# Kernel optimization log

Hardware: AMD Instinct MI355X
Metric: run time of the kernel (lower is better)

Reference implementation:

```python
import jax, jax.numpy as jnp
import numpy as np

N_NODES = 50000
N_EDGES = 1_600_000
IN_C, HID_C, OUT_C = 512, 256, 50
ALPHA = 0.1
NUM_LAYERS = 10


def setup_inputs() -> dict:
    key = jax.random.key(0)
    ks = jax.random.split(key, 8)
    x = jax.random.normal(ks[0], (N_NODES, IN_C), dtype=jnp.float32)
    edge_row = jax.random.randint(ks[1], (N_EDGES,), 0, N_NODES, dtype=jnp.int32)
    edge_col = jax.random.randint(ks[2], (N_EDGES,), 0, N_NODES, dtype=jnp.int32)
    edge_weight = jax.random.uniform(ks[3], (N_EDGES,), dtype=jnp.float32)
    s1 = 1.0 / np.sqrt(IN_C)
    s2 = 1.0 / np.sqrt(HID_C)
    W1 = jax.random.uniform(ks[4], (IN_C, HID_C), minval=-s1, maxval=s1, dtype=jnp.float32)
    b1 = jax.random.uniform(ks[5], (HID_C,), minval=-s1, maxval=s1, dtype=jnp.float32)
    W2 = jax.random.uniform(ks[6], (HID_C, OUT_C), minval=-s2, maxval=s2, dtype=jnp.float32)
    b2 = jax.random.uniform(ks[7], (OUT_C,), minval=-s2, maxval=s2, dtype=jnp.float32)
    return {"x": x, "edge_row": edge_row, "edge_col": edge_col,
            "edge_weight": edge_weight, "W1": W1, "b1": b1, "W2": W2, "b2": b2}


def reference(x, edge_row, edge_col, edge_weight, W1, b1, W2, b2):
    # MLP: Linear -> ReLU -> Linear (dropout inactive in eval, no batch norm)
    h = jax.nn.relu(x @ W1 + b1)          # [N, HID_C]
    h = h @ W2 + b2                        # [N, OUT_C]
    x0 = h

    def spmm(v):
        # out[i] = sum_{e: row[e]==i} w[e] * v[col[e]]
        msgs = v[edge_col] * edge_weight[:, None]   # [E, OUT_C]
        return jax.ops.segment_sum(msgs, edge_row, num_segments=N_NODES)

    def step(h, _):
        h = spmm(h) * (1.0 - ALPHA) + ALPHA * x0
        return h, None

    h, _ = jax.lax.scan(step, h, None, length=NUM_LAYERS)
    return jax.nn.log_softmax(h, axis=1)
```

## Files before the change

### kernel.cpp

```cpp
#include <hip/hip_runtime.h>
#include <cstddef>
#include <cstdint>
#include <math.h>

#define N_NODES 50000
#define N_EDGES 1600000
#define IN_C 512
#define HID_C 256
#define OUT_C 50
#define PAD_C 64
#define NUM_LAYERS 10
#define NBUCK 98
#define BSHIFT 9
#define BCAP 20480
#define PHB_CHUNK 8192
#define PHB_BLOCKS 196
#define AP 40

typedef __attribute__((ext_vector_type(8))) short short8;
typedef __attribute__((ext_vector_type(4))) float floatx4;

__device__ inline unsigned short f2bf(float f) {
    unsigned int u = __float_as_uint(f);
    u += 0x7fffu + ((u >> 16) & 1u);
    return (unsigned short)(u >> 16);
}

__global__ __launch_bounds__(256) void transpose_w1(const float* __restrict__ W1,
                                                    unsigned short* __restrict__ Wt) {
    __shared__ float tile[32][33];
    int bx = blockIdx.x;
    int by = blockIdx.y;
    int tx = threadIdx.x & 31, ty = threadIdx.x >> 5;
#pragma unroll
    for (int i = 0; i < 32; i += 8)
        tile[ty + i][tx] = W1[(bx * 32 + ty + i) * HID_C + by * 32 + tx];
    __syncthreads();
#pragma unroll
    for (int i = 0; i < 32; i += 8)
        Wt[(size_t)(by * 32 + ty + i) * IN_C + bx * 32 + tx] = f2bf(tile[tx][ty + i]);
}

__global__ __launch_bounds__(256) void gemm1_mfma(const float* __restrict__ A,
                                                  const unsigned short* __restrict__ Wt,
                                                  const float* __restrict__ bias,
                                                  float* __restrict__ C) {
    __shared__ unsigned short As[64 * AP];
    __shared__ unsigned short Bs[128 * AP];
    const int tid = threadIdx.x;
    const int wave = tid >> 6, lane = tid & 63;
    const int quad = lane >> 4, l16 = lane & 15;
    const int m0 = blockIdx.x * 64, n0 = blockIdx.y * 128;
    const int wm = (wave >> 1) * 32, wn = (wave & 1) * 64;

    floatx4 acc[2][4];
#pragma unroll
    for (int i = 0; i < 2; ++i)
#pragma unroll
        for (int j = 0; j < 4; ++j) acc[i][j] = (floatx4){0.f, 0.f, 0.f, 0.f};

    const int arow   = tid >> 2;
    const int achunk = (tid & 3) * 8;
    const int brow   = tid >> 1;
    const int bchunk = (tid & 1) * 16;

    float4 pa0[2], pa1[2];
    uint4  pb0[2], pb1[2];

    auto fetch = [&](int k0, float4* pa, uint4* pb) {
        int gr = m0 + arow;
        pa[0] = make_float4(0.f, 0.f, 0.f, 0.f);
        pa[1] = pa[0];
        if (gr < N_NODES) {
            const float* base = A + (size_t)gr * IN_C + k0 + achunk;
            pa[0] = *(const float4*)base;
            pa[1] = *(const float4*)(base + 4);
        }
        const unsigned short* wb = Wt + (size_t)(n0 + brow) * IN_C + k0 + bchunk;
        pb[0] = *(const uint4*)wb;
        pb[1] = *(const uint4*)(wb + 8);
    };
    auto stage = [&](const float4* pa, const uint4* pb) {
        ushort4 u1, u2;
        u1.x = f2bf(pa[0].x); u1.y = f2bf(pa[0].y); u1.z = f2bf(pa[0].z); u1.w = f2bf(pa[0].w);
        u2.x = f2bf(pa[1].x); u2.y = f2bf(pa[1].y); u2.z = f2bf(pa[1].z); u2.w = f2bf(pa[1].w);
        *(ushort4*)&As[arow * AP + achunk]     = u1;
        *(ushort4*)&As[arow * AP + achunk + 4] = u2;
        *(uint4*)&Bs[brow * AP + bchunk]     = pb[0];
        *(uint4*)&Bs[brow * AP + bchunk + 8] = pb[1];
    };
    auto mfma_phase = [&]() {
        short8 af[2], bf[4];
#pragma unroll
        for (int nt = 0; nt < 4; ++nt)
            bf[nt] = *(const short8*)&Bs[(wn + nt * 16 + l16) * AP + quad * 8];
#pragma unroll
        for (int mt = 0; mt < 2; ++mt)
            af[mt] = *(const short8*)&As[(wm + mt * 16 + l16) * AP + quad * 8];
#pragma unroll
        for (int mt = 0; mt < 2; ++mt)
#pragma unroll
            for (int nt = 0; nt < 4; ++nt)
                acc[mt][nt] = __builtin_amdgcn_mfma_f32_16x16x32_bf16(af[mt], bf[nt],
                                                                      acc[mt][nt], 0, 0, 0);
    };

    fetch(0, pa0, pb0);
    fetch(32, pa1, pb1);
    for (int k0 = 0; k0 < IN_C; k0 += 64) {
        __syncthreads();
        stage(pa0, pb0);
        __syncthreads();
        if (k0 + 64 < IN_C) fetch(k0 + 64, pa0, pb0);
        mfma_phase();
        __syncthreads();
        stage(pa1, pb1);
        __syncthreads();
        if (k0 + 96 < IN_C) fetch(k0 + 96, pa1, pb1);
        mfma_phase();
    }

#pragma unroll
    for (int nt = 0; nt < 4; ++nt) {
        int n = n0 + wn + nt * 16 + l16;
        float bn = bias[n];
#pragma unroll
        for (int mt = 0; mt < 2; ++mt) {
#pragma unroll
            for (int r = 0; r < 4; ++r) {
                int m = m0 + wm + mt * 16 + quad * 4 + r;
                if (m < N_NODES) {
                    float v = acc[mt][nt][r] + bn;
                    C[(size_t)m * HID_C + n] = v > 0.f ? v : 0.f;
                }
            }
        }
    }
}

__global__ void pad_w2(const float* __restrict__ W2, const float* __restrict__ b2,
                       float* __restrict__ Wp, float* __restrict__ bp) {
    int idx = blockIdx.x * blockDim.x + threadIdx.x;
    if (idx < HID_C * PAD_C) {
        int k = idx >> 6, j = idx & 63;
        Wp[idx] = (j < OUT_C) ? W2[k * OUT_C + j] : 0.f;
    }
    if (idx < PAD_C) bp[idx] = (idx < OUT_C) ? b2[idx] : 0.f;
}

__global__ __launch_bounds__(256) void gemm2_tiled(const float* __restrict__ H,
                                                   const float* __restrict__ Wp,
                                                   const float* __restrict__ bp,
                                                   float* __restrict__ h0f,
                                                   unsigned short* __restrict__ h0b) {
    __shared__ float As[16][68];
    __shared__ float Bs[16][64];
    const int tid = threadIdx.x;
    const int tx = tid & 15;
    const int ty = tid >> 4;
    const int m0 = blockIdx.x * 64;

    float acc[4][4];
#pragma unroll
    for (int i = 0; i < 4; ++i)
#pragma unroll
        for (int j = 0; j < 4; ++j) acc[i][j] = 0.f;

    const int arow = tid >> 2;
    const int akk  = (tid & 3) << 2;
    const int brow = tid >> 4;
    const int bcol = (tid & 15) << 2;

    for (int k0 = 0; k0 < HID_C; k0 += 16) {
        float4 av = make_float4(0.f, 0.f, 0.f, 0.f);
        int gr = m0 + arow;
        if (gr < N_NODES)
            av = *(const float4*)(H + (size_t)gr * HID_C + k0 + akk);
        As[akk + 0][arow] = av.x;
        As[akk + 1][arow] = av.y;
        As[akk + 2][arow] = av.z;
        As[akk + 3][arow] = av.w;
        float4 bv = *(const float4*)(Wp + (size_t)(k0 + brow) * PAD_C + bcol);
        *(float4*)&Bs[brow][bcol] = bv;
        __syncthreads();

#pragma unroll
        for (int kk = 0; kk < 16; ++kk) {
            float a[4], b[4];
#pragma unroll
            for (int i = 0; i < 4; ++i) a[i] = As[kk][ty * 4 + i];
#pragma unroll
            for (int j = 0; j < 4; ++j) b[j] = Bs[kk][tx * 4 + j];
#pragma unroll
            for (int i = 0; i < 4; ++i)
#pragma unroll
                for (int j = 0; j < 4; ++j) acc[i][j] = fmaf(a[i], b[j], acc[i][j]);
        }
        __syncthreads();
    }

#pragma unroll
    for (int i = 0; i < 4; ++i) {
        int r = m0 + ty * 4 + i;
        if (r >= N_NODES) continue;
#pragma unroll
        for (int j = 0; j < 4; ++j) {
            int c = tx * 4 + j;
            float v = acc[i][j] + bp[c];
            h0f[(size_t)r * PAD_C + c] = v;
            h0b[(size_t)r * PAD_C + c] = f2bf(v);
        }
    }
}

__global__ __launch_bounds__(256) void bucket_scatter(const int* __restrict__ erow,
                                                      const int* __restrict__ ecol,
                                                      const float* __restrict__ ew,
                                                      int* __restrict__ bfill,
                                                      uint2* __restrict__ buckets) {
    __shared__ int lcnt[NBUCK];
    __shared__ int lbase[NBUCK];
    const int t = threadIdx.x;
    for (int b = t; b < NBUCK; b += 256) lcnt[b] = 0;
    __syncthreads();
    const int e0 = blockIdx.x * PHB_CHUNK;
    const int e1 = min(e0 + PHB_CHUNK, N_EDGES);
    for (int e = e0 + t; e < e1; e += 256)
        atomicAdd(&lcnt[erow[e] >> BSHIFT], 1);
    __syncthreads();
    for (int b = t; b < NBUCK; b += 256) {
        lbase[b] = atomicAdd(&bfill[b], lcnt[b]);
        lcnt[b] = 0;
    }
    __syncthreads();
    for (int e = e0 + t; e < e1; e += 256) {
        int r = erow[e];
        int b = r >> BSHIFT;
        int o = atomicAdd(&lcnt[b], 1);
        int idx = lbase[b] + o;
        if (idx < BCAP) {
            unsigned packed = ((unsigned)(r - (b << BSHIFT)) << 17) | (unsigned)ecol[e];
            buckets[(size_t)b * BCAP + idx] = make_uint2(packed, __float_as_uint(ew[e]));
        }
    }
}

__global__ __launch_bounds__(128) void bucket_scan(const int* __restrict__ bfill,
                                                   int* __restrict__ bbase,
                                                   int* __restrict__ rowptr) {
    __shared__ int sd[128];
    int t = threadIdx.x;
    int v = (t < NBUCK) ? min(bfill[t], BCAP) : 0;
    sd[t] = v;
    __syncthreads();
    for (int off = 1; off < 128; off <<= 1) {
        int x = (t >= off) ? sd[t - off] : 0;
        __syncthreads();
        sd[t] += x;
        __syncthreads();
    }
    if (t < NBUCK) bbase[t] = sd[t] - v;
    if (t == NBUCK - 1) {
        bbase[NBUCK] = sd[t];
        rowptr[N_NODES] = sd[t];
    }
}

__global__ __launch_bounds__(256) void bucket_csr(const uint2* __restrict__ buckets,
                                                  const int* __restrict__ bfill,
                                                  const int* __restrict__ bbase,
                                                  int* __restrict__ rowptr,
                                                  uint2* __restrict__ edges) {
    __shared__ int hist[512];
    __shared__ int excl[512];
    __shared__ int psum[256];
    const int b = blockIdx.x;
    const int t = threadIdx.x;
    const int n = min(bfill[b], BCAP);
    const uint2* bk = buckets + (size_t)b * BCAP;

    hist[t] = 0; hist[t + 256] = 0;
    __syncthreads();
    for (int i = t; i < n; i += 256)
        atomicAdd(&hist[bk[i].x >> 17], 1);
    __syncthreads();
    int a0 = hist[2 * t], a1 = hist[2 * t + 1];
    psum[t] = a0 + a1;
    __syncthreads();
    for (int off = 1; off < 256; off <<= 1) {
        int x = (t >= off) ? psum[t - off] : 0;
        __syncthreads();
        psum[t] += x;
        __syncthreads();
    }
    int pe = psum[t] - (a0 + a1);
    excl[2 * t] = pe;
    excl[2 * t + 1] = pe + a0;
    __syncthreads();
    const int base = bbase[b];
#pragma unroll
    for (int k = 0; k < 2; ++k) {
        int lr = t + k * 256;
        int r = (b << BSHIFT) + lr;
        if (r < N_NODES) rowptr[r] = base + excl[lr];
    }
    hist[t] = 0; hist[t + 256] = 0;
    __syncthreads();
    for (int i = t; i < n; i += 256) {
        uint2 ed = bk[i];
        int lr = ed.x >> 17;
        int pos = base + excl[lr] + atomicAdd(&hist[lr], 1);
        edges[pos] = make_uint2(ed.x & 0x1FFFFu, ed.y);
    }
}

template <bool LAST>
__global__ __launch_bounds__(256) void prop8(const int* __restrict__ rowptr,
                                             const uint2* __restrict__ edges,
                                             const unsigned short* __restrict__ hin,
                                             const float* __restrict__ h0f,
                                             unsigned short* __restrict__ hout_b,
                                             float* __restrict__ out_f) {
    int wid = (blockIdx.x * blockDim.x + threadIdx.x) >> 6;
    if (wid >= N_NODES) return;
    int lane = threadIdx.x & 63;
    int slot = lane >> 3;
    int lc   = lane & 7;
    int s = rowptr[wid], e = rowptr[wid + 1];

    float acc0[8], acc1[8];
#pragma unroll
    for (int k = 0; k < 8; ++k) { acc0[k] = 0.f; acc1[k] = 0.f; }

    int i = s;
    for (; i + 16 <= e; i += 16) {
        uint2 cw0 = edges[i + slot];
        uint2 cw1 = edges[i + 8 + slot];
        uint4 hv0 = *(const uint4*)((const char*)hin + ((size_t)cw0.x << 7) + lc * 16);
        uint4 hv1 = *(const uint4*)((const char*)hin + ((size_t)cw1.x << 7) + lc * 16);
        float w0 = __uint_as_float(cw0.y);
        float w1 = __uint_as_float(cw1.y);
        acc0[0] = fmaf(w0, __uint_as_float(hv0.x << 16),         acc0[0]);
        acc0[1] = fmaf(w0, __uint_as_float(hv0.x & 0xffff0000u), acc0[1]);
        acc0[2] = fmaf(w0, __uint_as_float(hv0.y << 16),         acc0[2]);
        acc0[3] = fmaf(w0, __uint_as_float(hv0.y & 0xffff0000u), acc0[3]);
        acc0[4] = fmaf(w0, __uint_as_float(hv0.z << 16),         acc0[4]);
        acc0[5] = fmaf(w0, __uint_as_float(hv0.z & 0xffff0000u), acc0[5]);
        acc0[6] = fmaf(w0, __uint_as_float(hv0.w << 16),         acc0[6]);
        acc0[7] = fmaf(w0, __uint_as_float(hv0.w & 0xffff0000u), acc0[7]);
        acc1[0] = fmaf(w1, __uint_as_float(hv1.x << 16),         acc1[0]);
        acc1[1] = fmaf(w1, __uint_as_float(hv1.x & 0xffff0000u), acc1[1]);
        acc1[2] = fmaf(w1, __uint_as_float(hv1.y << 16),         acc1[2]);
        acc1[3] = fmaf(w1, __uint_as_float(hv1.y & 0xffff0000u), acc1[3]);
        acc1[4] = fmaf(w1, __uint_as_float(hv1.z << 16),         acc1[4]);
        acc1[5] = fmaf(w1, __uint_as_float(hv1.z & 0xffff0000u), acc1[5]);
        acc1[6] = fmaf(w1, __uint_as_float(hv1.w << 16),         acc1[6]);
        acc1[7] = fmaf(w1, __uint_as_float(hv1.w & 0xffff0000u), acc1[7]);
    }
    for (; i < e; i += 8) {
        int idx = i + slot;
        uint2 cw = (idx < e) ? edges[idx] : make_uint2(0u, 0u);
        float w  = (idx < e) ? __uint_as_float(cw.y) : 0.f;
        uint4 hv = *(const uint4*)((const char*)hin + ((size_t)cw.x << 7) + lc * 16);
        acc0[0] = fmaf(w, __uint_as_float(hv.x << 16),         acc0[0]);
        acc0[1] = fmaf(w, __uint_as_float(hv.x & 0xffff0000u), acc0[1]);
        acc0[2] = fmaf(w, __uint_as_float(hv.y << 16),         acc0[2]);
        acc0[3] = fmaf(w, __uint_as_float(hv.y & 0xffff0000u), acc0[3]);
        acc0[4] = fmaf(w, __uint_as_float(hv.z << 16),         acc0[4]);
        acc0[5] = fmaf(w, __uint_as_float(hv.z & 0xffff0000u), acc0[5]);
        acc0[6] = fmaf(w, __uint_as_float(hv.w << 16),         acc0[6]);
        acc0[7] = fmaf(w, __uint_as_float(hv.w & 0xffff0000u), acc0[7]);
    }

    float r[8];
#pragma unroll
    for (int k = 0; k < 8; ++k) {
        float v = acc0[k] + acc1[k];
        v += __shfl_xor(v, 8, 64);
        v += __shfl_xor(v, 16, 64);
        v += __shfl_xor(v, 32, 64);
        r[k] = v;
    }

    size_t off = (size_t)wid * PAD_C + lc * 8;
    float4 h0a = *(const float4*)(h0f + off);
    float4 h0b4 = *(const float4*)(h0f + off + 4);
    r[0] = 0.9f * r[0] + 0.1f * h0a.x;  r[1] = 0.9f * r[1] + 0.1f * h0a.y;
    r[2] = 0.9f * r[2] + 0.1f * h0a.z;  r[3] = 0.9f * r[3] + 0.1f * h0a.w;
    r[4] = 0.9f * r[4] + 0.1f * h0b4.x; r[5] = 0.9f * r[5] + 0.1f * h0b4.y;
    r[6] = 0.9f * r[6] + 0.1f * h0b4.z; r[7] = 0.9f * r[7] + 0.1f * h0b4.w;

    if (!LAST) {
        if (slot == 0) {
            uint4 u;
            u.x = ((unsigned)f2bf(r[1]) << 16) | f2bf(r[0]);
            u.y = ((unsigned)f2bf(r[3]) << 16) | f2bf(r[2]);
            u.z = ((unsigned)f2bf(r[5]) << 16) | f2bf(r[4]);
            u.w = ((unsigned)f2bf(r[7]) << 16) | f2bf(r[6]);
            *(uint4*)((char*)hout_b + ((size_t)wid << 7) + lc * 16) = u;
        }
    } else {
        int ch0 = lc * 8;
        float m = -INFINITY;
#pragma unroll
        for (int k = 0; k < 8; ++k) if (ch0 + k < OUT_C) m = fmaxf(m, r[k]);
        m = fmaxf(m, __shfl_xor(m, 1, 64));
        m = fmaxf(m, __shfl_xor(m, 2, 64));
        m = fmaxf(m, __shfl_xor(m, 4, 64));
        float ss = 0.f;
#pragma unroll
        for (int k = 0; k < 8; ++k) if (ch0 + k < OUT_C) ss += __expf(r[k] - m);
        ss += __shfl_xor(ss, 1, 64);
        ss += __shfl_xor(ss, 2, 64);
        ss += __shfl_xor(ss, 4, 64);
        float lse = __logf(ss);
        if (slot == 0) {
#pragma unroll
            for (int k = 0; k < 8; ++k)
                if (ch0 + k < OUT_C)
                    out_f[(size_t)wid * OUT_C + ch0 + k] = (r[k] - m) - lse;
        }
    }
}

extern "C" void kernel_launch(void* const* d_in, const int* in_sizes, int n_in,
                              void* d_out, int out_size, void* d_ws, size_t ws_size,
                              hipStream_t stream) {
    const float* x    = (const float*)d_in[0];
    const int*   erow = (const int*)d_in[1];
    const int*   ecol = (const int*)d_in[2];
    const float* ew   = (const float*)d_in[3];
    const float* W1   = (const float*)d_in[4];
    const float* b1   = (const float*)d_in[5];
    const float* W2   = (const float*)d_in[6];
    const float* b2   = (const float*)d_in[7];
    float* out = (float*)d_out;

    char* p = (char*)d_ws;
    auto alloc = [&](size_t bytes) {
        char* r = p;
        p += (bytes + 255) & ~(size_t)255;
        return r;
    };
    char*  h_hid_raw = alloc((size_t)N_NODES * HID_C * 4);
    float* h_hid  = (float*)h_hid_raw;
    float* h0f    = (float*)alloc((size_t)N_NODES * PAD_C * 4);
    unsigned short* h0b = (unsigned short*)alloc((size_t)N_NODES * PAD_C * 2);
    uint2* edges  = (uint2*)alloc((size_t)N_EDGES * 8);
    int*   rowptr = (int*)alloc((size_t)(N_NODES + 1) * 4);
    int*   bfill  = (int*)alloc((size_t)NBUCK * 4);
    int*   bbase  = (int*)alloc((size_t)(NBUCK + 1) * 4);
    float* Wp     = (float*)alloc((size_t)HID_C * PAD_C * 4);
    float* bp     = (float*)alloc((size_t)PAD_C * 4);
    unsigned short* Wt = (unsigned short*)alloc((size_t)HID_C * IN_C * 2);
    uint2* buckets = (uint2*)h_hid_raw;
    unsigned short* ha = (unsigned short*)h_hid_raw;
    unsigned short* hb = (unsigned short*)(h_hid_raw + (size_t)N_NODES * PAD_C * 2);

    hipMemsetAsync(bfill, 0, (size_t)NBUCK * 4, stream);

    bucket_scatter<<<PHB_BLOCKS, 256, 0, stream>>>(erow, ecol, ew, bfill, buckets);
    bucket_scan<<<1, 128, 0, stream>>>(bfill, bbase, rowptr);
    bucket_csr<<<NBUCK, 256, 0, stream>>>(buckets, bfill, bbase, rowptr, edges);

    transpose_w1<<<dim3(IN_C / 32, HID_C / 32), 256, 0, stream>>>(W1, Wt);
    gemm1_mfma<<<dim3((N_NODES + 63) / 64, HID_C / 128), 256, 0, stream>>>(x, Wt, b1, h_hid);
    pad_w2<<<(HID_C * PAD_C + 255) / 256, 256, 0, stream>>>(W2, b2, Wp, bp);
    gemm2_tiled<<<(N_NODES + 63) / 64, 256, 0, stream>>>(h_hid, Wp, bp, h0f, h0b);

    const int prop_blocks = (N_NODES * 64 + 255) / 256;
    const unsigned short* cur = h0b;
    unsigned short* nxt = ha;
    for (int l = 0; l < NUM_LAYERS - 1; ++l) {
        prop8<false><<<prop_blocks, 256, 0, stream>>>(rowptr, edges, cur, h0f,
                                                      nxt, nullptr);
        const unsigned short* t = nxt;
        nxt = (nxt == ha) ? hb : ha;
        cur = t;
    }
    prop8<true><<<prop_blocks, 256, 0, stream>>>(rowptr, edges, cur, h0f,
                                                 nullptr, out);
}
```

Before: 687.4 us.

## Use async global-to-LDS loads with full-N tiles in first GEMM

Rewrites the first GEMM to stage A (fp32, XOR-swizzled) and W1ᵀ tiles directly into double-buffered LDS with global_load_lds, instead of loading through registers. The bf16 conversion of A now happens at fragment-read time. Each block now covers all 256 output columns, so x is read once rather than twice. This trades more LDS use and per-wave accumulators (lower occupancy) for halved x traffic and less register staging. The async copy path depends on correct wait semantics, since only __syncthreads guards buffer reuse.

```diff
diff --git a/kernel.cpp b/kernel.cpp
--- a/kernel.cpp
+++ b/kernel.cpp
@@ -15,7 +15,6 @@
 #define BCAP 20480
 #define PHB_CHUNK 8192
 #define PHB_BLOCKS 196
-#define AP 40
 
 typedef __attribute__((ext_vector_type(8))) short short8;
 typedef __attribute__((ext_vector_type(4))) float floatx4;
@@ -25,6 +24,11 @@
     u += 0x7fffu + ((u >> 16) & 1u);
     return (unsigned short)(u >> 16);
 }
+
+#define ASYNC16(g, l)                                                     \
+    __builtin_amdgcn_global_load_lds(                                     \
+        (const __attribute__((address_space(1))) void*)(g),               \
+        (__attribute__((address_space(3))) void*)(l), 16, 0, 0)
 
 __global__ __launch_bounds__(256) void transpose_w1(const float* __restrict__ W1,
                                                     unsigned short* __restrict__ Wt) {
@@ -45,84 +49,81 @@
                                                   const unsigned short* __restrict__ Wt,
                                                   const float* __restrict__ bias,
                                                   float* __restrict__ C) {
-    __shared__ unsigned short As[64 * AP];
-    __shared__ unsigned short Bs[128 * AP];
-    const int tid = threadIdx.x;
+    __shared__ float          As[2][64 * 32];
+    __shared__ unsigned short Bs[2][256 * 32];
+    const int tid  = threadIdx.x;
     const int wave = tid >> 6, lane = tid & 63;
     const int quad = lane >> 4, l16 = lane & 15;
-    const int m0 = blockIdx.x * 64, n0 = blockIdx.y * 128;
-    const int wm = (wave >> 1) * 32, wn = (wave & 1) * 64;
-
-    floatx4 acc[2][4];
+    const int m0 = blockIdx.x * 64;
+    const int wm = (wave >> 1) * 32;
+    const int wn = (wave & 1) * 128;
+
+    floatx4 acc[2][8];
 #pragma unroll
     for (int i = 0; i < 2; ++i)
 #pragma unroll
-        for (int j = 0; j < 4; ++j) acc[i][j] = (floatx4){0.f, 0.f, 0.f, 0.f};
-
-    const int arow   = tid >> 2;
-    const int achunk = (tid & 3) * 8;
-    const int brow   = tid >> 1;
-    const int bchunk = (tid & 1) * 16;
-
-    float4 pa0[2], pa1[2];
-    uint4  pb0[2], pb1[2];
-
-    auto fetch = [&](int k0, float4* pa, uint4* pb) {
-        int gr = m0 + arow;
-        pa[0] = make_float4(0.f, 0.f, 0.f, 0.f);
-        pa[1] = pa[0];
-        if (gr < N_NODES) {
-            const float* base = A + (size_t)gr * IN_C + k0 + achunk;
-            pa[0] = *(const float4*)base;
-            pa[1] = *(const float4*)(base + 4);
-        }
-        const unsigned short* wb = Wt + (size_t)(n0 + brow) * IN_C + k0 + bchunk;
-        pb[0] = *(const uint4*)wb;
-        pb[1] = *(const uint4*)(wb + 8);
+        for (int j = 0; j < 8; ++j) acc[i][j] = (floatx4){0.f, 0.f, 0.f, 0.f};
+
+    auto stage = [&](int buf, int k0) {
+#pragma unroll
+        for (int j = 0; j < 2; ++j) {
+            int slot = tid + j * 256;
+            int r = slot >> 3, c = slot & 7;
+            int gr = m0 + r;
+            if (gr >= N_NODES) gr = N_NODES - 1;
+            const float* src = A + (size_t)gr * IN_C + k0 + ((c ^ (r & 7)) << 2);
+            ASYNC16(src, &As[buf][slot << 2]);
+        }
+#pragma unroll
+        for (int j = 0; j < 4; ++j) {
+            int slot = tid + j * 256;
+            int n = slot >> 2, c = slot & 3;
+            const unsigned short* src = Wt + (size_t)n * IN_C + k0 + (c << 3);
+            ASYNC16(src, &Bs[buf][slot << 3]);
+        }
     };
-    auto stage = [&](const float4* pa, const uint4* pb) {
-        ushort4 u1, u2;
-        u1.x = f2bf(pa[0].x); u1.y = f2bf(pa[0].y); u1.z = f2bf(pa[0].z); u1.w = f2bf(pa[0].w);
-        u2.x = f2bf(pa[1].x); u2.y = f2bf(pa[1].y); u2.z = f2bf(pa[1].z); u2.w = f2bf(pa[1].w);
-        *(ushort4*)&As[arow * AP + achunk]     = u1;
-        *(ushort4*)&As[arow * AP + achunk + 4] = u2;
-        *(uint4*)&Bs[brow * AP + bchunk]     = pb[0];
-        *(uint4*)&Bs[brow * AP + bchunk + 8] = pb[1];
-    };
-    auto mfma_phase = [&]() {
-        short8 af[2], bf[4];
-#pragma unroll
-        for (int nt = 0; nt < 4; ++nt)
-            bf[nt] = *(const short8*)&Bs[(wn + nt * 16 + l16) * AP + quad * 8];
+
+    auto compute = [&](int buf) {
+        short8 bfr[8], afr[2];
+#pragma unroll
+        for (int nt = 0; nt < 8; ++nt) {
+            int n = wn + nt * 16 + l16;
+            bfr[nt] = *(const short8*)&Bs[buf][(n << 5) + (quad << 3)];
+        }
+#pragma unroll
+        for (int mt = 0; mt < 2; ++mt) {
+            int r  = wm + mt * 16 + l16;
+            int rx = r & 7;
+            float4 lo = *(const float4*)&As[buf][(r << 5) + (((2 * quad)     ^ rx) << 2)];
+            float4 hi = *(const float4*)&As[buf][(r << 5) + (((2 * quad + 1) ^ rx) << 2)];
+            short8 a;
+            a[0] = (short)f2bf(lo.x); a[1] = (short)f2bf(lo.y);
+            a[2] = (short)f2bf(lo.z); a[3] = (short)f2bf(lo.w);
+            a[4] = (short)f2bf(hi.x); a[5] = (short)f2bf(hi.y);
+            a[6] = (short)f2bf(hi.z); a[7] = (short)f2bf(hi.w);
+            afr[mt] = a;
+        }
 #pragma unroll
         for (int mt = 0; mt < 2; ++mt)
-            af[mt] = *(const short8*)&As[(wm + mt * 16 + l16) * AP + quad * 8];
-#pragma unroll
-        for (int mt = 0; mt < 2; ++mt)
-#pragma unroll
-            for (int nt = 0; nt < 4; ++nt)
-                acc[mt][nt] = __builtin_amdgcn_mfma_f32_16x16x32_bf16(af[mt], bf[nt],
+#pragma unroll
+            for (int nt = 0; nt < 8; ++nt)
+                acc[mt][nt] = __builtin_amdgcn_mfma_f32_16x16x32_bf16(afr[mt], bfr[nt],
                                                                       acc[mt][nt], 0, 0, 0);
     };
 
-    fetch(0, pa0, pb0);
-    fetch(32, pa1, pb1);
-    for (int k0 = 0; k0 < IN_C; k0 += 64) {
-        __syncthreads();
-        stage(pa0, pb0);
-        __syncthreads();
-        if (k0 + 64 < IN_C) fetch(k0 + 64, pa0, pb0);
-        mfma_phase();
-        __syncthreads();
-        stage(pa1, pb1);
-        __syncthreads();
-        if (k0 + 96 < IN_C) fetch(k0 + 96, pa1, pb1);
-        mfma_phase();
-    }
-
-#pragma unroll
-    for (int nt = 0; nt < 4; ++nt) {
-        int n = n0 + wn + nt * 16 + l16;
+    stage(0, 0);
+    __syncthreads();
+    int buf = 0;
+    for (int ks = 0; ks < IN_C / 32; ++ks) {
+        if (ks + 1 < IN_C / 32) stage(buf ^ 1, (ks + 1) * 32);
+        compute(buf);
+        __syncthreads();
+        buf ^= 1;
+    }
+
+#pragma unroll
+    for (int nt = 0; nt < 8; ++nt) {
+        int n = wn + nt * 16 + l16;
         float bn = bias[n];
 #pragma unroll
         for (int mt = 0; mt < 2; ++mt) {
@@ -464,7 +465,7 @@
     bucket_csr<<<NBUCK, 256, 0, stream>>>(buckets, bfill, bbase, rowptr, edges);
 
     transpose_w1<<<dim3(IN_C / 32, HID_C / 32), 256, 0, stream>>>(W1, Wt);
-    gemm1_mfma<<<dim3((N_NODES + 63) / 64, HID_C / 128), 256, 0, stream>>>(x, Wt, b1, h_hid);
+    gemm1_mfma<<<dim3((N_NODES + 63) / 64), 256, 0, stream>>>(x, Wt, b1, h_hid);
     pad_w2<<<(HID_C * PAD_C + 255) / 256, 256, 0, stream>>>(W2, b2, Wp, bp);
     gemm2_tiled<<<(N_NODES + 63) / 64, 256, 0, stream>>>(h_hid, Wp, bp, h0f, h0b);
 
```

Result: faster. 645.8 us (-6.1%).
